# Kernel optimization log

Measured on AMD Instinct MI355X. Metric: run time of the kernel, lower is better.

The kernel has to match this reference:

```python
import jax, jax.numpy as jnp
import numpy as np

EPS = 1e-8


def _laplace_normalize(edge_row, edge_col, edge_vals, num_nodes):
    # D_r^{-1/2} A D_c^{-1/2} as in laplace_transform
    deg_r = jax.ops.segment_sum(edge_vals, edge_row, num_segments=num_nodes)
    deg_c = jax.ops.segment_sum(edge_vals, edge_col, num_segments=num_nodes)
    inv_r = 1.0 / (jnp.sqrt(deg_r) + EPS)
    inv_c = 1.0 / (jnp.sqrt(deg_c) + EPS)
    return edge_vals * inv_r[edge_row] * inv_c[edge_col]


def _l2norm(x):
    # F.normalize(p=2, dim=1): x / max(||x||, eps) with eps=1e-12
    n = jnp.sqrt(jnp.sum(x * x, axis=1, keepdims=True))
    return x / jnp.maximum(n, 1e-12)


def setup_inputs() -> dict:
    key = jax.random.key(0)
    k1, k2, k3, k4, k5, k6 = jax.random.split(key, 6)
    N, D, E, B = 100000, 64, 3200000, 4096
    node_features = jax.random.normal(k1, (N, D), dtype=jnp.float32)
    edge_row = jax.random.randint(k2, (E,), 0, N, dtype=jnp.int32)
    edge_col = jax.random.randint(k3, (E,), 0, N, dtype=jnp.int32)
    edge_vals = jnp.ones((E,), dtype=jnp.float32)
    a_id = jax.random.randint(k4, (B,), 0, N, dtype=jnp.int32)
    pos_id = jax.random.randint(k5, (B,), 0, N, dtype=jnp.int32)
    neg_id = jax.random.randint(k6, (B,), 0, N, dtype=jnp.int32)
    return {"node_features": node_features, "edge_row": edge_row,
            "edge_col": edge_col, "edge_vals": edge_vals,
            "a_id": a_id, "pos_id": pos_id, "neg_id": neg_id}


def reference(node_features, edge_row, edge_col, edge_vals, a_id, pos_id, neg_id):
    num_nodes = node_features.shape[0]
    num_layers = 3
    norm_vals = _laplace_normalize(edge_row, edge_col, edge_vals, num_nodes)

    # one_propagate: repeated spmm + per-layer L2 normalize, mean over layers
    features = node_features
    acc = node_features  # layer-0 term of the running sum (not normalized)
    for _ in range(num_layers):
        msgs = norm_vals[:, None] * features[edge_col]  # [E, D]
        features = jax.ops.segment_sum(msgs, edge_row, num_segments=num_nodes)
        acc = acc + _l2norm(features)
    node_rep = acc / (num_layers + 1)

    # BPR loss over batch
    a = node_rep[a_id]
    pos_pred = jnp.sum(a * node_rep[pos_id], axis=1)
    neg_pred = jnp.sum(a * node_rep[neg_id], axis=1)
    loss = jnp.mean(-jax.nn.log_sigmoid(pos_pred - neg_pred))
    return loss
```

## Files before the change

### kernel.cpp

```cpp
#include <hip/hip_runtime.h>
#include <math.h>

#define DDIM 64
#define BUCKET 1024
#define LRSHIFT 17
#define CMASK 0x1FFFF
#define LRMASK 0x3FF
#define NBLK 512
#define TPB_BIN 512
#define TPB_CP 512
#define MAXNB 128

typedef unsigned long long ull;
typedef _Float16 half2_t __attribute__((ext_vector_type(2)));

__device__ inline unsigned int bf16_hi(float v) {
    unsigned int a = __float_as_uint(v);
    return (a + 0x7fffu + ((a >> 16) & 1u)) & 0xffff0000u;
}

__device__ inline unsigned int pk_f16x2(float lo, float hi) {
    return __builtin_bit_cast(unsigned int, __builtin_amdgcn_cvt_pkrtz(lo, hi));
}

__device__ inline half2_t dup_lo16(unsigned int s) {
    return __builtin_bit_cast(half2_t, __builtin_amdgcn_perm(0u, s, 0x01000100u));
}

__global__ void init_fill_kernel(int* __restrict__ gfill_r, int* __restrict__ gfill_c,
                                 int NB, int cap) {
    int k = blockIdx.x * blockDim.x + threadIdx.x;
    if (k < NB) {
        gfill_r[k * 16] = k * cap;
        gfill_c[k * 16] = k * cap;
    }
}

__global__ __launch_bounds__(TPB_BIN)
void binning_kernel(const int* __restrict__ erow, const int* __restrict__ ecol,
                    const float* __restrict__ evals,
                    int* __restrict__ gfill_r, int* __restrict__ gfill_c,
                    ull* __restrict__ br, unsigned int* __restrict__ bc,
                    int E, int NB, int chunk) {
    __shared__ int hr[8][MAXNB];
    __shared__ int hc[8][MAXNB];
    __shared__ int fr[MAXNB];
    __shared__ int fc[MAXNB];
    int t = threadIdx.x;
    int wv = t >> 6;
    for (int k = t; k < 8 * MAXNB; k += TPB_BIN) { (&hr[0][0])[k] = 0; (&hc[0][0])[k] = 0; }
    __syncthreads();
    int lo = blockIdx.x * chunk;
    int hi = min(E, lo + chunk);
    int nq = (hi - lo) >> 2;
    int rem = (hi - lo) & 3;
    for (int p = t; p < nq; p += TPB_BIN) {
        int i = lo + 4 * p;
        int4 r4 = *(const int4*)(erow + i);
        int4 c4 = *(const int4*)(ecol + i);
        atomicAdd(&hr[wv][r4.x >> 10], 1);
        atomicAdd(&hr[wv][r4.y >> 10], 1);
        atomicAdd(&hr[wv][r4.z >> 10], 1);
        atomicAdd(&hr[wv][r4.w >> 10], 1);
        atomicAdd(&hc[wv][c4.x >> 10], 1);
        atomicAdd(&hc[wv][c4.y >> 10], 1);
        atomicAdd(&hc[wv][c4.z >> 10], 1);
        atomicAdd(&hc[wv][c4.w >> 10], 1);
    }
    if (t == 0) {
        for (int i = hi - rem; i < hi; i++) {
            atomicAdd(&hr[0][erow[i] >> 10], 1);
            atomicAdd(&hc[0][ecol[i] >> 10], 1);
        }
    }
    __syncthreads();
    if (t < NB) {
        int sr = 0, sc = 0;
        #pragma unroll
        for (int w2 = 0; w2 < 8; w2++) { sr += hr[w2][t]; sc += hc[w2][t]; }
        fr[t] = atomicAdd(&gfill_r[t * 16], sr);
        fc[t] = atomicAdd(&gfill_c[t * 16], sc);
    }
    __syncthreads();
    for (int p = t; p < nq; p += TPB_BIN) {
        int i = lo + 4 * p;
        int4 r4 = *(const int4*)(erow + i);
        int4 c4 = *(const int4*)(ecol + i);
        float4 v4 = *(const float4*)(evals + i);
        int pos0 = atomicAdd(&fr[r4.x >> 10], 1);
        int pos1 = atomicAdd(&fr[r4.y >> 10], 1);
        int pos2 = atomicAdd(&fr[r4.z >> 10], 1);
        int pos3 = atomicAdd(&fr[r4.w >> 10], 1);
        br[pos0] = ((ull)__float_as_uint(v4.x) << 32) | ((ull)(r4.x & 1023) << LRSHIFT) | (unsigned)c4.x;
        br[pos1] = ((ull)__float_as_uint(v4.y) << 32) | ((ull)(r4.y & 1023) << LRSHIFT) | (unsigned)c4.y;
        br[pos2] = ((ull)__float_as_uint(v4.z) << 32) | ((ull)(r4.z & 1023) << LRSHIFT) | (unsigned)c4.z;
        br[pos3] = ((ull)__float_as_uint(v4.w) << 32) | ((ull)(r4.w & 1023) << LRSHIFT) | (unsigned)c4.w;
        int q0 = atomicAdd(&fc[c4.x >> 10], 1);
        int q1 = atomicAdd(&fc[c4.y >> 10], 1);
        int q2 = atomicAdd(&fc[c4.z >> 10], 1);
        int q3 = atomicAdd(&fc[c4.w >> 10], 1);
        bc[q0] = bf16_hi(v4.x) | (unsigned)(c4.x & 1023);
        bc[q1] = bf16_hi(v4.y) | (unsigned)(c4.y & 1023);
        bc[q2] = bf16_hi(v4.z) | (unsigned)(c4.z & 1023);
        bc[q3] = bf16_hi(v4.w) | (unsigned)(c4.w & 1023);
    }
    if (t == 0) {
        for (int i = hi - rem; i < hi; i++) {
            int r = erow[i], c = ecol[i];
            float v = evals[i];
            int pos = atomicAdd(&fr[r >> 10], 1);
            br[pos] = ((ull)__float_as_uint(v) << 32) | ((ull)(r & 1023) << LRSHIFT) | (unsigned)c;
            int pos2 = atomicAdd(&fc[c >> 10], 1);
            bc[pos2] = bf16_hi(v) | (unsigned)(c & 1023);
        }
    }
}

__global__ __launch_bounds__(TPB_CP)
void count_kernel(const ull* __restrict__ br, const unsigned int* __restrict__ bc,
                  const int* __restrict__ gfill_r, const int* __restrict__ gfill_c,
                  int* __restrict__ subcnt, float* __restrict__ subds,
                  float* __restrict__ subdsc, int cap) {
    __shared__ int cnt[BUCKET];
    __shared__ float ds[BUCKET];
    __shared__ float dsc[BUCKET];
    int b = blockIdx.x >> 3, ch = blockIdx.x & 7;
    int t = threadIdx.x;
    for (int k = t; k < BUCKET; k += TPB_CP) { cnt[k] = 0; ds[k] = 0.0f; dsc[k] = 0.0f; }
    __syncthreads();
    int s = b * cap;
    int e = gfill_r[b * 16];
    int len = ((((e - s) + 7) >> 3) + 1) & ~1;
    int cs = s + ch * len, ce = min(e, cs + len);
    int m = cs + ((ce - cs) & ~1);
    for (int i = cs + 2 * t; i < m; i += 2 * TPB_CP) {
        ull p0 = br[i];
        ull p1 = br[i + 1];
        int lr0 = (int)((p0 >> LRSHIFT) & LRMASK);
        int lr1 = (int)((p1 >> LRSHIFT) & LRMASK);
        atomicAdd(&cnt[lr0], 1);
        atomicAdd(&cnt[lr1], 1);
        atomicAdd(&ds[lr0], __uint_as_float((unsigned)(p0 >> 32)));
        atomicAdd(&ds[lr1], __uint_as_float((unsigned)(p1 >> 32)));
    }
    if (t == 0 && m < ce) {
        ull p = br[m];
        int lr = (int)((p >> LRSHIFT) & LRMASK);
        atomicAdd(&cnt[lr], 1);
        atomicAdd(&ds[lr], __uint_as_float((unsigned)(p >> 32)));
    }
    int e2 = gfill_c[b * 16];
    int len2 = ((((e2 - s) + 7) >> 3) + 1) & ~1;
    int cs2 = s + ch * len2, ce2 = min(e2, cs2 + len2);
    int m2 = cs2 + ((ce2 - cs2) & ~1);
    for (int i = cs2 + 2 * t; i < m2; i += 2 * TPB_CP) {
        uint2 p = *(const uint2*)(bc + i);
        atomicAdd(&dsc[p.x & 0x3FFu], __uint_as_float(p.x & 0xffff0000u));
        atomicAdd(&dsc[p.y & 0x3FFu], __uint_as_float(p.y & 0xffff0000u));
    }
    if (t == 0 && m2 < ce2) {
        unsigned int p = bc[m2];
        atomicAdd(&dsc[p & 0x3FFu], __uint_as_float(p & 0xffff0000u));
    }
    __syncthreads();
    size_t base = ((size_t)b * 8 + ch) * BUCKET;
    for (int k = t; k < BUCKET; k += TPB_CP) {
        subcnt[base + k] = cnt[k];
        subds[base + k]  = ds[k];
        subdsc[base + k] = dsc[k];
    }
}

__global__ __launch_bounds__(1024)
void combine_kernel(int* __restrict__ subcnt, const float* __restrict__ subds,
                    const float* __restrict__ subdsc,
                    int* __restrict__ rowstart, int* __restrict__ rowend,
                    float* __restrict__ inv_r, float* __restrict__ inv_c,
                    int N, int cap) {
    __shared__ int tot[BUCKET];
    int b = blockIdx.x, t = threadIdx.x;
    size_t base = (size_t)b * 8 * BUCKET;
    int c8[8];
    int sum = 0;
    #pragma unroll
    for (int c = 0; c < 8; c++) { c8[c] = subcnt[base + c * BUCKET + t]; sum += c8[c]; }
    int sum2 = (sum + 1) & ~1;
    tot[t] = sum2;
    __syncthreads();
    for (int off = 1; off < BUCKET; off <<= 1) {
        int v = (t >= off) ? tot[t - off] : 0;
        __syncthreads();
        tot[t] += v;
        __syncthreads();
    }
    int excl = tot[t] - sum2;
    int node = b * BUCKET + t;
    int s = b * cap;
    if (node < N) {
        rowstart[node] = s + excl;
        rowend[node]   = s + excl + sum;
    }
    int run = s + excl;
    #pragma unroll
    for (int c = 0; c < 8; c++) { int v = c8[c]; subcnt[base + c * BUCKET + t] = run; run += v; }
    float d = 0.0f, dc = 0.0f;
    #pragma unroll
    for (int c = 0; c < 8; c++) { d += subds[base + c * BUCKET + t]; dc += subdsc[base + c * BUCKET + t]; }
    inv_r[b * BUCKET + t] = 1.0f / (sqrtf(d) + 1e-8f);
    inv_c[b * BUCKET + t] = 1.0f / (sqrtf(dc) + 1e-8f);
}

__global__ __launch_bounds__(TPB_CP)
void place_kernel(const ull* __restrict__ br, const int* __restrict__ gfill_r,
                  const int* __restrict__ pbase, const float* __restrict__ inv_r,
                  const float* __restrict__ inv_c,
                  unsigned int* __restrict__ cw, int cap) {
    __shared__ int fill[BUCKET];
    __shared__ float irs[BUCKET];
    int b = blockIdx.x >> 3, ch = blockIdx.x & 7;
    int t = threadIdx.x;
    size_t pb = ((size_t)b * 8 + ch) * BUCKET;
    for (int k = t; k < BUCKET; k += TPB_CP) {
        fill[k] = pbase[pb + k];
        irs[k]  = inv_r[b * BUCKET + k];
    }
    __syncthreads();
    int s = b * cap;
    int e = gfill_r[b * 16];
    int len = ((((e - s) + 7) >> 3) + 1) & ~1;
    int cs = s + ch * len, ce = min(e, cs + len);
    int m = cs + ((ce - cs) & ~1);
    for (int i = cs + 2 * t; i < m; i += 2 * TPB_CP) {
        ull p0 = br[i];
        ull p1 = br[i + 1];
        int c0 = (int)(p0 & CMASK), c1 = (int)(p1 & CMASK);
        int lr0 = (int)((p0 >> LRSHIFT) & LRMASK);
        int lr1 = (int)((p1 >> LRSHIFT) & LRMASK);
        float v0 = __uint_as_float((unsigned)(p0 >> 32));
        float v1 = __uint_as_float((unsigned)(p1 >> 32));
        int pos0 = atomicAdd(&fill[lr0], 1);
        int pos1 = atomicAdd(&fill[lr1], 1);
        float w0 = v0 * inv_c[c0] * irs[lr0];
        float w1 = v1 * inv_c[c1] * irs[lr1];
        cw[pos0] = ((unsigned)c0 << 15) | ((pk_f16x2(w0, w0) & 0xFFFFu) >> 1);
        cw[pos1] = ((unsigned)c1 << 15) | ((pk_f16x2(w1, w1) & 0xFFFFu) >> 1);
    }
    if (t == 0 && m < ce) {
        ull p = br[m];
        int c = (int)(p & CMASK);
        int lr = (int)((p >> LRSHIFT) & LRMASK);
        float v = __uint_as_float((unsigned)(p >> 32));
        int pos = atomicAdd(&fill[lr], 1);
        float wv = v * inv_c[c] * irs[lr];
        cw[pos] = ((unsigned)c << 15) | ((pk_f16x2(wv, wv) & 0xFFFFu) >> 1);
    }
}

__global__ void cvt_kernel(const float* __restrict__ src, unsigned int* __restrict__ acc16,
                           unsigned int* __restrict__ dst, long n4) {
    long i = (long)blockIdx.x * blockDim.x + threadIdx.x;
    if (i < n4) {
        float4 v = ((const float4*)src)[i];
        uint2 o;
        o.x = pk_f16x2(v.x, v.y);
        o.y = pk_f16x2(v.z, v.w);
        ((uint2*)acc16)[i] = o;
        ((uint2*)dst)[i] = o;
    }
}

__global__ __launch_bounds__(256)
void spmm_f16_kernel(const int* __restrict__ rowstart, const int* __restrict__ rowend,
                     const unsigned int* __restrict__ cw,
                     const unsigned short* __restrict__ fin,
                     unsigned short* __restrict__ fout,
                     unsigned short* __restrict__ acc16, int N, int writeOut) {
    int wid = blockIdx.x * (blockDim.x >> 6) + (threadIdx.x >> 6);
    if (wid >= N) return;
    int lane = threadIdx.x & 63;
    int g = lane >> 3;
    int h = lane & 7;
    int s = rowstart[wid], e = rowend[wid];
    half2_t a2[8];
    #pragma unroll
    for (int k = 0; k < 8; k++) a2[k] = (half2_t)0;

    int nfull = (e - s) >> 4;
    int base = s;
    for (int it = 0; it < nfull; it++, base += 16) {
        int j0 = base + 2 * g;
        uint2 pw = *(const uint2*)(cw + j0);
        int c0 = (int)(pw.x >> 15);
        int c1 = (int)(pw.y >> 15);
        uint4 q0 = ((const uint4*)(fin + ((long)c0 << 6)))[h];
        uint4 q1 = ((const uint4*)(fin + ((long)c1 << 6)))[h];
        half2_t w0 = dup_lo16(pw.x << 1);
        half2_t w1 = dup_lo16(pw.y << 1);
        a2[0] += w0 * __builtin_bit_cast(half2_t, q0.x);
        a2[1] += w0 * __builtin_bit_cast(half2_t, q0.y);
        a2[2] += w0 * __builtin_bit_cast(half2_t, q0.z);
        a2[3] += w0 * __builtin_bit_cast(half2_t, q0.w);
        a2[4] += w1 * __builtin_bit_cast(half2_t, q1.x);
        a2[5] += w1 * __builtin_bit_cast(half2_t, q1.y);
        a2[6] += w1 * __builtin_bit_cast(half2_t, q1.z);
        a2[7] += w1 * __builtin_bit_cast(half2_t, q1.w);
    }
    if (base < e) {
        int j0 = base + 2 * g, j1 = j0 + 1;
        uint2 pw = *(const uint2*)(cw + j0);
        int c0 = (int)(pw.x >> 15);
        int c1 = (int)(pw.y >> 15);
        half2_t w0 = (j0 < e) ? dup_lo16(pw.x << 1) : (half2_t)0;
        half2_t w1 = (j1 < e) ? dup_lo16(pw.y << 1) : (half2_t)0;
        uint4 q0 = ((const uint4*)(fin + ((long)c0 << 6)))[h];
        uint4 q1 = ((const uint4*)(fin + ((long)c1 << 6)))[h];
        a2[0] += w0 * __builtin_bit_cast(half2_t, q0.x);
        a2[1] += w0 * __builtin_bit_cast(half2_t, q0.y);
        a2[2] += w0 * __builtin_bit_cast(half2_t, q0.z);
        a2[3] += w0 * __builtin_bit_cast(half2_t, q0.w);
        a2[4] += w1 * __builtin_bit_cast(half2_t, q1.x);
        a2[5] += w1 * __builtin_bit_cast(half2_t, q1.y);
        a2[6] += w1 * __builtin_bit_cast(half2_t, q1.z);
        a2[7] += w1 * __builtin_bit_cast(half2_t, q1.w);
    }

    float a[8];
    #pragma unroll
    for (int k = 0; k < 4; k++) {
        a[2 * k]     = (float)a2[k][0] + (float)a2[k + 4][0];
        a[2 * k + 1] = (float)a2[k][1] + (float)a2[k + 4][1];
    }
    #pragma unroll
    for (int k = 0; k < 8; k++) {
        a[k] += __shfl_xor(a[k], 8);
        a[k] += __shfl_xor(a[k], 16);
        a[k] += __shfl_xor(a[k], 32);
    }
    float ss = 0.0f;
    #pragma unroll
    for (int k = 0; k < 8; k++) ss += a[k] * a[k];
    ss += __shfl_xor(ss, 1);
    ss += __shfl_xor(ss, 2);
    ss += __shfl_xor(ss, 4);
    float s2 = 1.0f / fmaxf(sqrtf(ss), 1e-12f);
    if (g == 0) {
        uint4 o;
        o.x = pk_f16x2(a[0], a[1]);
        o.y = pk_f16x2(a[2], a[3]);
        o.z = pk_f16x2(a[4], a[5]);
        o.w = pk_f16x2(a[6], a[7]);
        if (writeOut) ((uint4*)(fout + ((long)wid << 6)))[h] = o;
        uint4* ap = (uint4*)(acc16 + ((long)wid << 6)) + h;
        uint4 old = *ap;
        uint4 inc;
        inc.x = pk_f16x2(a[0] * s2, a[1] * s2);
        inc.y = pk_f16x2(a[2] * s2, a[3] * s2);
        inc.z = pk_f16x2(a[4] * s2, a[5] * s2);
        inc.w = pk_f16x2(a[6] * s2, a[7] * s2);
        uint4 nw;
        nw.x = __builtin_bit_cast(unsigned int, __builtin_bit_cast(half2_t, old.x) + __builtin_bit_cast(half2_t, inc.x));
        nw.y = __builtin_bit_cast(unsigned int, __builtin_bit_cast(half2_t, old.y) + __builtin_bit_cast(half2_t, inc.y));
        nw.z = __builtin_bit_cast(unsigned int, __builtin_bit_cast(half2_t, old.z) + __builtin_bit_cast(half2_t, inc.z));
        nw.w = __builtin_bit_cast(unsigned int, __builtin_bit_cast(half2_t, old.w) + __builtin_bit_cast(half2_t, inc.w));
        *ap = nw;
    }
}

__global__ void loss_terms_kernel(const unsigned short* __restrict__ acc16,
                                  const int* __restrict__ a_id, const int* __restrict__ p_id,
                                  const int* __restrict__ n_id,
                                  float* __restrict__ terms, int B) {
    long gid = (long)blockIdx.x * blockDim.x + threadIdx.x;
    int b = (int)(gid >> 6);
    int lane = threadIdx.x & 63;
    if (b < B) {
        int ia = a_id[b], ip = p_id[b], in2 = n_id[b];
        float a = (float)__builtin_bit_cast(_Float16, acc16[(long)ia * DDIM + lane]);
        float p = (float)__builtin_bit_cast(_Float16, acc16[(long)ip * DDIM + lane]);
        float n = (float)__builtin_bit_cast(_Float16, acc16[(long)in2 * DDIM + lane]);
        float dp = a * p, dn = a * n;
        #pragma unroll
        for (int off = 1; off < 64; off <<= 1) { dp += __shfl_xor(dp, off); dn += __shfl_xor(dn, off); }
        if (lane == 0) {
            float x = (dp - dn) * 0.0625f;
            terms[b] = fmaxf(-x, 0.0f) + log1pf(expf(-fabsf(x)));
        }
    }
}

__global__ void reduce_kernel(const float* __restrict__ terms, float* __restrict__ out, int B) {
    __shared__ float sm[256];
    float s = 0.0f;
    for (int i = threadIdx.x; i < B; i += 256) s += terms[i];
    sm[threadIdx.x] = s;
    __syncthreads();
    for (int stride = 128; stride > 0; stride >>= 1) {
        if (threadIdx.x < stride) sm[threadIdx.x] += sm[threadIdx.x + stride];
        __syncthreads();
    }
    if (threadIdx.x == 0) out[0] = sm[0] / (float)B;
}

extern "C" void kernel_launch(void* const* d_in, const int* in_sizes, int n_in,
                              void* d_out, int out_size, void* d_ws, size_t ws_size,
                              hipStream_t stream) {
    const float* nf    = (const float*)d_in[0];
    const int*   erow  = (const int*)d_in[1];
    const int*   ecol  = (const int*)d_in[2];
    const float* evals = (const float*)d_in[3];
    const int*   a_id  = (const int*)d_in[4];
    const int*   p_id  = (const int*)d_in[5];
    const int*   n_id  = (const int*)d_in[6];

    int N = in_sizes[0] / DDIM;
    int E = in_sizes[1];
    int B = in_sizes[4];
    int NB = (N + BUCKET - 1) / BUCKET;
    int chunk = (((E + NBLK - 1) / NBLK) + 3) & ~3;
    int Npad = NB * BUCKET;

    long capl = ((long)E * BUCKET) / N;
    int cap = (int)(capl + capl / 12 + 2048);
    cap = (cap + 63) & ~63;

    size_t regionA = (size_t)cap * NB * 8;
    size_t regionB = (size_t)cap * NB * 4;
    size_t featB16 = (size_t)N * DDIM * 2;
    size_t subBytes = (size_t)NB * 8 * BUCKET * 4;

    char* w = (char*)d_ws;
    ull*  br     = (ull*)w;
    char* regAp  = w;                 w += regionA;
    unsigned int* bc = (unsigned int*)w;
    unsigned int* cw = (unsigned int*)w;  w += regionB + 64;
    unsigned int* acc16 = (unsigned int*)w;  w += featB16;
    int* subcnt  = (int*)w;           w += subBytes;
    float* subds = (float*)w;         w += subBytes;
    float* subdsc= (float*)w;         w += subBytes;
    float* inv_c = (float*)w;         w += (size_t)Npad * 4;
    float* inv_r = (float*)w;         w += (size_t)Npad * 4;
    int* rowstart= (int*)w;           w += (size_t)N * 4;
    int* rowend  = (int*)w;           w += (size_t)N * 4;
    int* gfill_r = (int*)w;           w += (size_t)NB * 16 * 4;
    int* gfill_c = (int*)w;           w += (size_t)NB * 16 * 4;
    float* terms = (float*)w;         w += (size_t)B * 4;

    unsigned short* fb0 = (unsigned short*)regAp;
    unsigned short* fb1 = (unsigned short*)(regAp + featB16);

    init_fill_kernel<<<1, 128, 0, stream>>>(gfill_r, gfill_c, NB, cap);
    binning_kernel<<<NBLK, TPB_BIN, 0, stream>>>(erow, ecol, evals, gfill_r, gfill_c,
                                                 br, bc, E, NB, chunk);
    count_kernel<<<NB * 8, TPB_CP, 0, stream>>>(br, bc, gfill_r, gfill_c,
                                                subcnt, subds, subdsc, cap);
    combine_kernel<<<NB, 1024, 0, stream>>>(subcnt, subds, subdsc, rowstart, rowend,
                                            inv_r, inv_c, N, cap);
    place_kernel<<<NB * 8, TPB_CP, 0, stream>>>(br, gfill_r, subcnt, inv_r, inv_c, cw, cap);

    long n4 = (long)N * DDIM / 4;
    cvt_kernel<<<(unsigned)((n4 + 255) / 256), 256, 0, stream>>>(nf, acc16, (unsigned int*)fb0, n4);

    unsigned spmmGrid = (unsigned)((N + 3) / 4);
    spmm_f16_kernel<<<spmmGrid, 256, 0, stream>>>(rowstart, rowend, cw, fb0, fb1,
                                                  (unsigned short*)acc16, N, 1);
    spmm_f16_kernel<<<spmmGrid, 256, 0, stream>>>(rowstart, rowend, cw, fb1, fb0,
                                                  (unsigned short*)acc16, N, 1);
    spmm_f16_kernel<<<spmmGrid, 256, 0, stream>>>(rowstart, rowend, cw, fb0, fb1,
                                                  (unsigned short*)acc16, N, 0);

    loss_terms_kernel<<<(unsigned)(((long)B * 64 + 255) / 256), 256, 0, stream>>>(
        (const unsigned short*)acc16, a_id, p_id, n_id, terms, B);
    reduce_kernel<<<1, 256, 0, stream>>>(terms, (float*)d_out, B);
}
```

Before: 425.1 us.

## Split row-bucket records into key and bf16 value arrays, per-wave bucket offsets

The row-binned edge records shrink from 8-byte packed entries to a 4-byte key plus a 2-byte bf16 value, cutting scatter and re-read traffic in the binning, count and place kernels. The binning kernel grows to 1024 threads (16 waves), and each wave now gets its own prefix-summed slot range per bucket, so the scatter phase uses per-wave LDS atomics instead of one contended shared counter. Edge values are rounded to bf16 before degree summation and weight calculation, which loses precision for non-unit values. The workspace layout is adjusted so the feature buffers still fit in region A.

```diff
diff --git a/kernel.cpp b/kernel.cpp
--- a/kernel.cpp
+++ b/kernel.cpp
@@ -3,20 +3,28 @@
 
 #define DDIM 64
 #define BUCKET 1024
-#define LRSHIFT 17
 #define CMASK 0x1FFFF
-#define LRMASK 0x3FF
 #define NBLK 512
-#define TPB_BIN 512
+#define TPB_BIN 1024
+#define NWV 16
 #define TPB_CP 512
 #define MAXNB 128
 
 typedef unsigned long long ull;
 typedef _Float16 half2_t __attribute__((ext_vector_type(2)));
+
+__device__ inline unsigned short bf16_of(float v) {
+    unsigned int a = __float_as_uint(v);
+    return (unsigned short)((a + 0x7fffu + ((a >> 16) & 1u)) >> 16);
+}
 
 __device__ inline unsigned int bf16_hi(float v) {
     unsigned int a = __float_as_uint(v);
     return (a + 0x7fffu + ((a >> 16) & 1u)) & 0xffff0000u;
+}
+
+__device__ inline float bf16_to_f(unsigned int bits16) {
+    return __uint_as_float(bits16 << 16);
 }
 
 __device__ inline unsigned int pk_f16x2(float lo, float hi) {
@@ -40,15 +48,16 @@
 void binning_kernel(const int* __restrict__ erow, const int* __restrict__ ecol,
                     const float* __restrict__ evals,
                     int* __restrict__ gfill_r, int* __restrict__ gfill_c,
-                    ull* __restrict__ br, unsigned int* __restrict__ bc,
+                    unsigned int* __restrict__ brk, unsigned short* __restrict__ brv,
+                    unsigned int* __restrict__ bc,
                     int E, int NB, int chunk) {
-    __shared__ int hr[8][MAXNB];
-    __shared__ int hc[8][MAXNB];
+    __shared__ int hr[NWV][MAXNB];
+    __shared__ int hc[NWV][MAXNB];
     __shared__ int fr[MAXNB];
     __shared__ int fc[MAXNB];
     int t = threadIdx.x;
     int wv = t >> 6;
-    for (int k = t; k < 8 * MAXNB; k += TPB_BIN) { (&hr[0][0])[k] = 0; (&hc[0][0])[k] = 0; }
+    for (int k = t; k < NWV * MAXNB; k += TPB_BIN) { (&hr[0][0])[k] = 0; (&hc[0][0])[k] = 0; }
     __syncthreads();
     int lo = blockIdx.x * chunk;
     int hi = min(E, lo + chunk);
@@ -77,9 +86,15 @@
     if (t < NB) {
         int sr = 0, sc = 0;
         #pragma unroll
-        for (int w2 = 0; w2 < 8; w2++) { sr += hr[w2][t]; sc += hc[w2][t]; }
-        fr[t] = atomicAdd(&gfill_r[t * 16], sr);
-        fc[t] = atomicAdd(&gfill_c[t * 16], sc);
+        for (int w2 = 0; w2 < NWV; w2++) { sr += hr[w2][t]; sc += hc[w2][t]; }
+        int basr = atomicAdd(&gfill_r[t * 16], sr);
+        int basc = atomicAdd(&gfill_c[t * 16], sc);
+        fr[t] = basr; fc[t] = basc;
+        #pragma unroll
+        for (int w2 = 0; w2 < NWV; w2++) {
+            int a = hr[w2][t]; hr[w2][t] = basr; basr += a;
+            int b = hc[w2][t]; hc[w2][t] = basc; basc += b;
+        }
     }
     __syncthreads();
     for (int p = t; p < nq; p += TPB_BIN) {
@@ -87,18 +102,22 @@
         int4 r4 = *(const int4*)(erow + i);
         int4 c4 = *(const int4*)(ecol + i);
         float4 v4 = *(const float4*)(evals + i);
-        int pos0 = atomicAdd(&fr[r4.x >> 10], 1);
-        int pos1 = atomicAdd(&fr[r4.y >> 10], 1);
-        int pos2 = atomicAdd(&fr[r4.z >> 10], 1);
-        int pos3 = atomicAdd(&fr[r4.w >> 10], 1);
-        br[pos0] = ((ull)__float_as_uint(v4.x) << 32) | ((ull)(r4.x & 1023) << LRSHIFT) | (unsigned)c4.x;
-        br[pos1] = ((ull)__float_as_uint(v4.y) << 32) | ((ull)(r4.y & 1023) << LRSHIFT) | (unsigned)c4.y;
-        br[pos2] = ((ull)__float_as_uint(v4.z) << 32) | ((ull)(r4.z & 1023) << LRSHIFT) | (unsigned)c4.z;
-        br[pos3] = ((ull)__float_as_uint(v4.w) << 32) | ((ull)(r4.w & 1023) << LRSHIFT) | (unsigned)c4.w;
-        int q0 = atomicAdd(&fc[c4.x >> 10], 1);
-        int q1 = atomicAdd(&fc[c4.y >> 10], 1);
-        int q2 = atomicAdd(&fc[c4.z >> 10], 1);
-        int q3 = atomicAdd(&fc[c4.w >> 10], 1);
+        int pos0 = atomicAdd(&hr[wv][r4.x >> 10], 1);
+        int pos1 = atomicAdd(&hr[wv][r4.y >> 10], 1);
+        int pos2 = atomicAdd(&hr[wv][r4.z >> 10], 1);
+        int pos3 = atomicAdd(&hr[wv][r4.w >> 10], 1);
+        brk[pos0] = ((unsigned)(r4.x & 1023) << 17) | (unsigned)c4.x;
+        brk[pos1] = ((unsigned)(r4.y & 1023) << 17) | (unsigned)c4.y;
+        brk[pos2] = ((unsigned)(r4.z & 1023) << 17) | (unsigned)c4.z;
+        brk[pos3] = ((unsigned)(r4.w & 1023) << 17) | (unsigned)c4.w;
+        brv[pos0] = bf16_of(v4.x);
+        brv[pos1] = bf16_of(v4.y);
+        brv[pos2] = bf16_of(v4.z);
+        brv[pos3] = bf16_of(v4.w);
+        int q0 = atomicAdd(&hc[wv][c4.x >> 10], 1);
+        int q1 = atomicAdd(&hc[wv][c4.y >> 10], 1);
+        int q2 = atomicAdd(&hc[wv][c4.z >> 10], 1);
+        int q3 = atomicAdd(&hc[wv][c4.w >> 10], 1);
         bc[q0] = bf16_hi(v4.x) | (unsigned)(c4.x & 1023);
         bc[q1] = bf16_hi(v4.y) | (unsigned)(c4.y & 1023);
         bc[q2] = bf16_hi(v4.z) | (unsigned)(c4.z & 1023);
@@ -108,16 +127,18 @@
         for (int i = hi - rem; i < hi; i++) {
             int r = erow[i], c = ecol[i];
             float v = evals[i];
-            int pos = atomicAdd(&fr[r >> 10], 1);
-            br[pos] = ((ull)__float_as_uint(v) << 32) | ((ull)(r & 1023) << LRSHIFT) | (unsigned)c;
-            int pos2 = atomicAdd(&fc[c >> 10], 1);
+            int pos = atomicAdd(&hr[0][r >> 10], 1);
+            brk[pos] = ((unsigned)(r & 1023) << 17) | (unsigned)c;
+            brv[pos] = bf16_of(v);
+            int pos2 = atomicAdd(&hc[0][c >> 10], 1);
             bc[pos2] = bf16_hi(v) | (unsigned)(c & 1023);
         }
     }
 }
 
 __global__ __launch_bounds__(TPB_CP)
-void count_kernel(const ull* __restrict__ br, const unsigned int* __restrict__ bc,
+void count_kernel(const unsigned int* __restrict__ brk, const unsigned short* __restrict__ brv,
+                  const unsigned int* __restrict__ bc,
                   const int* __restrict__ gfill_r, const int* __restrict__ gfill_c,
                   int* __restrict__ subcnt, float* __restrict__ subds,
                   float* __restrict__ subdsc, int cap) {
@@ -134,20 +155,20 @@
     int cs = s + ch * len, ce = min(e, cs + len);
     int m = cs + ((ce - cs) & ~1);
     for (int i = cs + 2 * t; i < m; i += 2 * TPB_CP) {
-        ull p0 = br[i];
-        ull p1 = br[i + 1];
-        int lr0 = (int)((p0 >> LRSHIFT) & LRMASK);
-        int lr1 = (int)((p1 >> LRSHIFT) & LRMASK);
+        uint2 k2 = *(const uint2*)(brk + i);
+        unsigned int v2 = *(const unsigned int*)(brv + i);
+        int lr0 = (int)(k2.x >> 17);
+        int lr1 = (int)(k2.y >> 17);
         atomicAdd(&cnt[lr0], 1);
         atomicAdd(&cnt[lr1], 1);
-        atomicAdd(&ds[lr0], __uint_as_float((unsigned)(p0 >> 32)));
-        atomicAdd(&ds[lr1], __uint_as_float((unsigned)(p1 >> 32)));
+        atomicAdd(&ds[lr0], bf16_to_f(v2 & 0xFFFFu));
+        atomicAdd(&ds[lr1], bf16_to_f(v2 >> 16));
     }
     if (t == 0 && m < ce) {
-        ull p = br[m];
-        int lr = (int)((p >> LRSHIFT) & LRMASK);
+        unsigned int k = brk[m];
+        int lr = (int)(k >> 17);
         atomicAdd(&cnt[lr], 1);
-        atomicAdd(&ds[lr], __uint_as_float((unsigned)(p >> 32)));
+        atomicAdd(&ds[lr], bf16_to_f((unsigned int)brv[m]));
     }
     int e2 = gfill_c[b * 16];
     int len2 = ((((e2 - s) + 7) >> 3) + 1) & ~1;
@@ -211,7 +232,8 @@
 }
 
 __global__ __launch_bounds__(TPB_CP)
-void place_kernel(const ull* __restrict__ br, const int* __restrict__ gfill_r,
+void place_kernel(const unsigned int* __restrict__ brk, const unsigned short* __restrict__ brv,
+                  const int* __restrict__ gfill_r,
                   const int* __restrict__ pbase, const float* __restrict__ inv_r,
                   const float* __restrict__ inv_c,
                   unsigned int* __restrict__ cw, int cap) {
@@ -231,13 +253,13 @@
     int cs = s + ch * len, ce = min(e, cs + len);
     int m = cs + ((ce - cs) & ~1);
     for (int i = cs + 2 * t; i < m; i += 2 * TPB_CP) {
-        ull p0 = br[i];
-        ull p1 = br[i + 1];
-        int c0 = (int)(p0 & CMASK), c1 = (int)(p1 & CMASK);
-        int lr0 = (int)((p0 >> LRSHIFT) & LRMASK);
-        int lr1 = (int)((p1 >> LRSHIFT) & LRMASK);
-        float v0 = __uint_as_float((unsigned)(p0 >> 32));
-        float v1 = __uint_as_float((unsigned)(p1 >> 32));
+        uint2 k2 = *(const uint2*)(brk + i);
+        unsigned int v2 = *(const unsigned int*)(brv + i);
+        int c0 = (int)(k2.x & CMASK), c1 = (int)(k2.y & CMASK);
+        int lr0 = (int)(k2.x >> 17);
+        int lr1 = (int)(k2.y >> 17);
+        float v0 = bf16_to_f(v2 & 0xFFFFu);
+        float v1 = bf16_to_f(v2 >> 16);
         int pos0 = atomicAdd(&fill[lr0], 1);
         int pos1 = atomicAdd(&fill[lr1], 1);
         float w0 = v0 * inv_c[c0] * irs[lr0];
@@ -246,10 +268,10 @@
         cw[pos1] = ((unsigned)c1 << 15) | ((pk_f16x2(w1, w1) & 0xFFFFu) >> 1);
     }
     if (t == 0 && m < ce) {
-        ull p = br[m];
-        int c = (int)(p & CMASK);
-        int lr = (int)((p >> LRSHIFT) & LRMASK);
-        float v = __uint_as_float((unsigned)(p >> 32));
+        unsigned int k = brk[m];
+        int c = (int)(k & CMASK);
+        int lr = (int)(k >> 17);
+        float v = bf16_to_f((unsigned int)brv[m]);
         int pos = atomicAdd(&fill[lr], 1);
         float wv = v * inv_c[c] * irs[lr];
         cw[pos] = ((unsigned)c << 15) | ((pk_f16x2(wv, wv) & 0xFFFFu) >> 1);
@@ -423,14 +445,18 @@
     int cap = (int)(capl + capl / 12 + 2048);
     cap = (cap + 63) & ~63;
 
-    size_t regionA = (size_t)cap * NB * 8;
+    size_t brkBytes = (size_t)cap * NB * 4;
+    size_t brvBytes = (size_t)cap * NB * 2;
+    size_t featB16 = (size_t)N * DDIM * 2;
+    size_t regionA = brkBytes + brvBytes;
+    if (regionA < 2 * featB16) regionA = 2 * featB16;
     size_t regionB = (size_t)cap * NB * 4;
-    size_t featB16 = (size_t)N * DDIM * 2;
     size_t subBytes = (size_t)NB * 8 * BUCKET * 4;
 
     char* w = (char*)d_ws;
-    ull*  br     = (ull*)w;
     char* regAp  = w;                 w += regionA;
+    unsigned int* brk = (unsigned int*)regAp;
+    unsigned short* brv = (unsigned short*)(regAp + brkBytes);
     unsigned int* bc = (unsigned int*)w;
     unsigned int* cw = (unsigned int*)w;  w += regionB + 64;
     unsigned int* acc16 = (unsigned int*)w;  w += featB16;
@@ -450,12 +476,12 @@
 
     init_fill_kernel<<<1, 128, 0, stream>>>(gfill_r, gfill_c, NB, cap);
     binning_kernel<<<NBLK, TPB_BIN, 0, stream>>>(erow, ecol, evals, gfill_r, gfill_c,
-                                                 br, bc, E, NB, chunk);
-    count_kernel<<<NB * 8, TPB_CP, 0, stream>>>(br, bc, gfill_r, gfill_c,
+                                                 brk, brv, bc, E, NB, chunk);
+    count_kernel<<<NB * 8, TPB_CP, 0, stream>>>(brk, brv, bc, gfill_r, gfill_c,
                                                 subcnt, subds, subdsc, cap);
     combine_kernel<<<NB, 1024, 0, stream>>>(subcnt, subds, subdsc, rowstart, rowend,
                                             inv_r, inv_c, N, cap);
-    place_kernel<<<NB * 8, TPB_CP, 0, stream>>>(br, gfill_r, subcnt, inv_r, inv_c, cw, cap);
+    place_kernel<<<NB * 8, TPB_CP, 0, stream>>>(brk, brv, gfill_r, subcnt, inv_r, inv_c, cw, cap);
 
     long n4 = (long)N * DDIM / 4;
     cvt_kernel<<<(unsigned)((n4 + 255) / 256), 256, 0, stream>>>(nf, acc16, (unsigned int*)fb0, n4);
```

Result: no change. 424.4 us (-0.2%).
